# Kernel tuning notes

Hardware: AMD Instinct MI355X
Metric: run time of the kernel (lower is better)

Reference implementation:

```python
import jax, jax.numpy as jnp
import numpy as np

N, E = 50000, 800000
IN, C, H, EDIM = 128, 16, 8, 8  # in_channels, out_channels per head, heads, edge_dim
NEG_SLOPE = 0.2


def setup_inputs() -> dict:
    key = jax.random.key(0)
    ks = jax.random.split(key, 10)
    g = 1.0 / np.sqrt(IN)
    inp = {
        "x": jax.random.normal(ks[0], (N, IN), dtype=jnp.float32),
        "edge_index": jax.random.randint(ks[1], (2, E), 0, N, dtype=jnp.int64),
        "edge_attr": jax.random.normal(ks[2], (E, EDIM), dtype=jnp.float32),
        # GATv2Conv params (share_weights=False): lin_l, lin_r with bias, lin_edge no bias
        "W_l": jax.random.normal(ks[3], (IN, H * C), dtype=jnp.float32) * g,
        "b_l": jnp.zeros((H * C,), dtype=jnp.float32),
        "W_r": jax.random.normal(ks[4], (IN, H * C), dtype=jnp.float32) * g,
        "b_r": jnp.zeros((H * C,), dtype=jnp.float32),
        "W_e": jax.random.normal(ks[5], (EDIM, H * C), dtype=jnp.float32) * (1.0 / np.sqrt(EDIM)),
        "att": jax.random.normal(ks[6], (H, C), dtype=jnp.float32) * (1.0 / np.sqrt(C)),
        "bias": jnp.zeros((H * C,), dtype=jnp.float32),
    }
    return inp


def _gatv2_forward(x, edge_index, edge_attr, W_l, b_l, W_r, b_r, W_e, att, bias):
    n = x.shape[0]
    x_l = (x @ W_l + b_l).reshape(n, H, C)  # source transform
    x_r = (x @ W_r + b_r).reshape(n, H, C)  # target transform

    # add self-loops; edge_attr fill_value='mean' (PyG GATv2Conv default)
    loop = jnp.arange(n, dtype=edge_index.dtype)
    src = jnp.concatenate([edge_index[0], loop])
    dst = jnp.concatenate([edge_index[1], loop])
    loop_attr = jnp.broadcast_to(edge_attr.mean(axis=0, keepdims=True), (n, EDIM))
    e_attr = jnp.concatenate([edge_attr, loop_attr], axis=0)  # [E+N, EDIM]

    e_emb = (e_attr @ W_e).reshape(-1, H, C)  # [E+N, H, C]
    m = x_l[src] + x_r[dst] + e_emb          # gather per edge
    m = jax.nn.leaky_relu(m, NEG_SLOPE)
    logit = jnp.einsum("ehc,hc->eh", m, att)  # [E+N, H]

    # destination-grouped (scatter) softmax
    seg_max = jax.ops.segment_max(logit, dst, num_segments=n)
    expd = jnp.exp(logit - seg_max[dst])
    seg_sum = jax.ops.segment_sum(expd, dst, num_segments=n)
    alpha = expd / (seg_sum[dst] + 1e-16)     # [E+N, H]

    msg = alpha[:, :, None] * x_l[src]        # [E+N, H, C]
    out = jax.ops.segment_sum(msg, dst, num_segments=n)  # [N, H, C]
    return out.reshape(n, H * C) + bias       # concat heads + bias


def reference(x, edge_index, edge_attr, W_l, b_l, W_r, b_r, W_e, att, bias):
    return _gatv2_forward(x, edge_index, edge_attr, W_l, b_l, W_r, b_r, W_e, att, bias)
```

## Files before the change

kernel.cpp:

```cpp
#include <hip/hip_runtime.h>

#define NHEAD 8
#define CH    16
#define HC    128
#define INC   128
#define EDIM  8
#define NEG   0.2f

typedef _Float16 h8 __attribute__((ext_vector_type(8)));
typedef _Float16 h4 __attribute__((ext_vector_type(4)));
typedef _Float16 h2 __attribute__((ext_vector_type(2)));
typedef float    f4 __attribute__((ext_vector_type(4)));

__device__ __forceinline__ float lrelu(float v) { return v > 0.f ? v : NEG * v; }

__global__ void k_loop_emb(const float* __restrict__ attr_sum, const float* __restrict__ We,
                           const float* __restrict__ att, float* __restrict__ loop_emb,
                           _Float16* __restrict__ We16, _Float16* __restrict__ att16,
                           float invE) {
    int j = threadIdx.x;
    float acc = 0.f;
    #pragma unroll
    for (int d = 0; d < EDIM; ++d) {
        float w = We[d * HC + j];
        acc += attr_sum[d] * invE * w;
        We16[d * HC + j] = (_Float16)w;
    }
    loop_emb[j] = acc;
    att16[j] = (_Float16)att[j];
}

__global__ void k_packW(const float* __restrict__ Wl, const float* __restrict__ Wr,
                        _Float16* __restrict__ packed) {
    int id = blockIdx.x * blockDim.x + threadIdx.x;
    int l  = id & 63;
    int kb = (id >> 6) & 3;
    int t  = id >> 8;
    int col = t * 16 + (l & 15);
    const float* W = (col < HC) ? Wl : Wr;
    int c = col & 127;
    int kbase = kb * 32 + (l >> 4) * 8;
    _Float16* dst = packed + (size_t)id * 8;
    #pragma unroll
    for (int j = 0; j < 8; ++j) dst[j] = (_Float16)W[(size_t)(kbase + j) * HC + c];
}

__global__ __launch_bounds__(256) void k_gemm_mfma(
        const float* __restrict__ x, const _Float16* __restrict__ packed,
        const float* __restrict__ bl, const float* __restrict__ br,
        _Float16* __restrict__ xh, int N) {
    __shared__ _Float16 st[16][264];
    int nb0 = blockIdx.x * 128;
    int w  = threadIdx.x >> 6;
    int l  = threadIdx.x & 63;

    const h8* pk = (const h8*)packed;
    h8 bfrag[4][4];
    #pragma unroll
    for (int t4 = 0; t4 < 4; ++t4)
        #pragma unroll
        for (int kb = 0; kb < 4; ++kb)
            bfrag[t4][kb] = pk[(size_t)(((w * 4 + t4) * 4 + kb) * 64 + l)];

    float bv[4];
    int cl = l & 15;
    #pragma unroll
    for (int t4 = 0; t4 < 4; ++t4) {
        int col = w * 64 + t4 * 16 + cl;
        bv[t4] = (col < HC) ? bl[col] : br[col - HC];
    }

    int g = l >> 4;
    int r0 = g * 4;
    for (int mt = 0; mt < 8; ++mt) {
        int m0 = nb0 + mt * 16;
        if (m0 >= N) break;
        int row = m0 + cl; if (row >= N) row = N - 1;
        const float* xp = x + (size_t)row * INC + g * 8;
        h8 afrag[4];
        #pragma unroll
        for (int kb = 0; kb < 4; ++kb) {
            float4 u = *(const float4*)(xp + kb * 32);
            float4 v = *(const float4*)(xp + kb * 32 + 4);
            h8 a;
            a[0] = (_Float16)u.x; a[1] = (_Float16)u.y; a[2] = (_Float16)u.z; a[3] = (_Float16)u.w;
            a[4] = (_Float16)v.x; a[5] = (_Float16)v.y; a[6] = (_Float16)v.z; a[7] = (_Float16)v.w;
            afrag[kb] = a;
        }
        f4 acc[4];
        #pragma unroll
        for (int t4 = 0; t4 < 4; ++t4) { f4 z = {0.f, 0.f, 0.f, 0.f}; acc[t4] = z; }
        #pragma unroll
        for (int kb = 0; kb < 4; ++kb)
            #pragma unroll
            for (int t4 = 0; t4 < 4; ++t4)
                acc[t4] = __builtin_amdgcn_mfma_f32_16x16x32_f16(afrag[kb], bfrag[t4][kb], acc[t4], 0, 0, 0);
        #pragma unroll
        for (int t4 = 0; t4 < 4; ++t4) {
            int col = w * 64 + t4 * 16 + cl;
            #pragma unroll
            for (int j = 0; j < 4; ++j)
                st[r0 + j][col] = (_Float16)(acc[t4][j] + bv[t4]);
        }
        __syncthreads();
        #pragma unroll
        for (int q = 0; q < 2; ++q) {
            int cch = threadIdx.x + 256 * q;
            int r = cch >> 5, ch = (cch & 31) * 8;
            int node = m0 + r;
            if (node < N) *(h8*)(xh + (size_t)node * 256 + ch) = *(const h8*)&st[r][ch];
        }
        __syncthreads();
    }
}

__global__ void k_hist(const int* __restrict__ ei, int* __restrict__ cnt,
                       int* __restrict__ rank, int E) {
    int t = blockIdx.x * blockDim.x + threadIdx.x;
    if (t < E) rank[t] = atomicAdd(&cnt[ei[E + t]], 1);
}

__global__ void k_scan1(const int* __restrict__ cnt, int* __restrict__ off,
                        int* __restrict__ bsum, int N) {
    __shared__ int wpre[16];
    int i = blockIdx.x * 1024 + threadIdx.x;
    int lane = threadIdx.x & 63, wid = threadIdx.x >> 6;
    int v = (i < N) ? cnt[i] : 0;
    int s = v;
    #pragma unroll
    for (int d = 1; d < 64; d <<= 1) {
        int t = __shfl_up(s, d);
        if (lane >= d) s += t;
    }
    if (lane == 63) wpre[wid] = s;
    __syncthreads();
    if (threadIdx.x == 0) {
        int run = 0;
        #pragma unroll
        for (int q = 0; q < 16; ++q) { int t = wpre[q]; wpre[q] = run; run += t; }
        bsum[blockIdx.x] = run;
    }
    __syncthreads();
    if (i <= N) off[i] = wpre[wid] + s - v;
}

__global__ void k_scan2(const int* __restrict__ bsum, int* __restrict__ bsx, int nb) {
    int lane = threadIdx.x;
    int v = (lane < nb) ? bsum[lane] : 0;
    int s = v;
    #pragma unroll
    for (int d = 1; d < 64; d <<= 1) {
        int t = __shfl_up(s, d);
        if (lane >= d) s += t;
    }
    if (lane < nb) bsx[lane] = s - v;
}

__global__ void k_scatter(const int* __restrict__ ei, const float* __restrict__ ea,
                          const int* __restrict__ off, const int* __restrict__ bsx,
                          const int* __restrict__ rank,
                          int* __restrict__ esrc, h8* __restrict__ eac,
                          float* __restrict__ attr_sum, int E) {
    __shared__ float red[4][8];
    int t = blockIdx.x * blockDim.x + threadIdx.x;
    float av[8] = {0.f, 0.f, 0.f, 0.f, 0.f, 0.f, 0.f, 0.f};
    if (t < E) {
        int dst = ei[E + t];
        int pos = off[dst] + bsx[dst >> 10] + rank[t];
        esrc[pos] = ei[t];
        float4 a0 = *(const float4*)(ea + (size_t)t * EDIM);
        float4 a1 = *(const float4*)(ea + (size_t)t * EDIM + 4);
        av[0] = a0.x; av[1] = a0.y; av[2] = a0.z; av[3] = a0.w;
        av[4] = a1.x; av[5] = a1.y; av[6] = a1.z; av[7] = a1.w;
        h8 v;
        #pragma unroll
        for (int k = 0; k < 8; ++k) v[k] = (_Float16)av[k];
        eac[pos] = v;
    }
    #pragma unroll
    for (int m = 1; m < 64; m <<= 1) {
        #pragma unroll
        for (int k = 0; k < 8; ++k) av[k] += __shfl_xor(av[k], m);
    }
    int lane = threadIdx.x & 63, wid = threadIdx.x >> 6;
    if (lane == 0) {
        #pragma unroll
        for (int k = 0; k < 8; ++k) red[wid][k] = av[k];
    }
    __syncthreads();
    if (threadIdx.x < 8) {
        float s = red[0][threadIdx.x] + red[1][threadIdx.x] + red[2][threadIdx.x] + red[3][threadIdx.x];
        atomicAdd(&attr_sum[threadIdx.x], s);
    }
}

__global__ void k_gather(const int* __restrict__ esrc, const h8* __restrict__ eac,
                         const _Float16* __restrict__ We16, const _Float16* __restrict__ att16,
                         const float* __restrict__ att,
                         const _Float16* __restrict__ xh,
                         const float* __restrict__ loop_emb, const float* __restrict__ bias,
                         const int* __restrict__ off, const int* __restrict__ bsx,
                         float* __restrict__ out, int N) {
    int wave = (blockIdx.x * blockDim.x + threadIdx.x) >> 6;
    int lane = threadIdx.x & 63;
    if (wave >= N) return;
    int dst = __builtin_amdgcn_readfirstlane(wave);
    int half = lane >> 5;
    int l = lane & 31;
    int c0 = l * 4;

    h4 we4[EDIM];
    #pragma unroll
    for (int d = 0; d < EDIM; ++d) we4[d] = *(const h4*)(We16 + d * HC + c0);
    h2 attlo = *(const h2*)(att16 + c0);
    h2 atthi = *(const h2*)(att16 + c0 + 2);
    h4 xr4 = *(const h4*)(xh + (size_t)dst * 256 + HC + c0);
    float xr0 = (float)xr4[0], xr1 = (float)xr4[1], xr2f = (float)xr4[2], xr3 = (float)xr4[3];

    float acc0 = 0.f, acc1 = 0.f, acc2 = 0.f, acc3 = 0.f, segw = 0.f;

    {
        h4 xl4 = *(const h4*)(xh + (size_t)dst * 256 + c0);
        float x0 = (float)xl4[0], x1 = (float)xl4[1], x2 = (float)xl4[2], x3 = (float)xl4[3];
        float4 le = *(const float4*)(loop_emb + c0);
        float4 af = *(const float4*)(att + c0);
        float m0 = lrelu(x0 + xr0 + le.x);
        float m1 = lrelu(x1 + xr1 + le.y);
        float m2 = lrelu(x2 + xr2f + le.z);
        float m3 = lrelu(x3 + xr3 + le.w);
        float p = m0 * af.x + m1 * af.y + m2 * af.z + m3 * af.w;
        p += __shfl_xor(p, 1); p += __shfl_xor(p, 2);
        float w = half ? 0.f : __expf(p);
        segw += w; acc0 += w * x0; acc1 += w * x1; acc2 += w * x2; acc3 += w * x3;
    }

    int beg = off[dst] + bsx[dst >> 10];
    int end = off[dst + 1] + bsx[(dst + 1) >> 10];
    if (beg < end) {
        const h4 z4 = {};
        h4 ng4; ng4[0] = (_Float16)NEG; ng4[1] = (_Float16)NEG; ng4[2] = (_Float16)NEG; ng4[3] = (_Float16)NEG;
        int last = end - 1;
        int j0 = beg + half;     if (j0 > last) j0 = last;
        int j1 = beg + 2 + half; if (j1 > last) j1 = last;
        int j2 = beg + 4 + half; if (j2 > last) j2 = last;
        int sA = esrc[j0]; h8 aA = eac[j0];
        int sB = esrc[j1]; h8 aB = eac[j1];
        int sC = esrc[j2]; h8 aC = eac[j2];
        h4 xlA = *(const h4*)(xh + (size_t)sA * 256 + c0);
        h4 xlB = *(const h4*)(xh + (size_t)sB * 256 + c0);
        for (int i = beg; i < end; i += 2) {
            h4 xlC = *(const h4*)(xh + (size_t)sC * 256 + c0);
            int j3 = i + 6 + half; if (j3 > last) j3 = last;
            int sD = esrc[j3]; h8 aD = eac[j3];
            bool valid = (i + half) < end;
            h4 e4 = {};
            #pragma unroll
            for (int d = 0; d < EDIM; ++d) {
                h4 ad; ad[0] = aA[d]; ad[1] = aA[d]; ad[2] = aA[d]; ad[3] = aA[d];
                e4 += ad * we4[d];
            }
            h4 m4 = xlA + xr4 + e4;
            h4 mp = __builtin_elementwise_max(m4, z4);
            h4 mn = __builtin_elementwise_min(m4, z4);
            m4 = mp + mn * ng4;
            h2 mlo; mlo[0] = m4[0]; mlo[1] = m4[1];
            h2 mhi; mhi[0] = m4[2]; mhi[1] = m4[3];
#if __has_builtin(__builtin_amdgcn_fdot2)
            float p = __builtin_amdgcn_fdot2(mlo, attlo, 0.f, false);
            p = __builtin_amdgcn_fdot2(mhi, atthi, p, false);
#else
            float p = (float)m4[0] * (float)attlo[0] + (float)m4[1] * (float)attlo[1]
                    + (float)m4[2] * (float)atthi[0] + (float)m4[3] * (float)atthi[1];
#endif
            p += __shfl_xor(p, 1);
            p += __shfl_xor(p, 2);
            float w = valid ? __expf(p) : 0.f;
            segw += w;
            acc0 += w * (float)xlA[0];
            acc1 += w * (float)xlA[1];
            acc2 += w * (float)xlA[2];
            acc3 += w * (float)xlA[3];
            aA = aB; aB = aC; aC = aD;
            xlA = xlB; xlB = xlC;
            sC = sD;
        }
    }

    segw += __shfl_xor(segw, 32);
    acc0 += __shfl_xor(acc0, 32);
    acc1 += __shfl_xor(acc1, 32);
    acc2 += __shfl_xor(acc2, 32);
    acc3 += __shfl_xor(acc3, 32);

    if (half == 0) {
        float inv = 1.f / (segw + 1e-16f);
        float4 bv = *(const float4*)(bias + c0);
        float4 o;
        o.x = acc0 * inv + bv.x;
        o.y = acc1 * inv + bv.y;
        o.z = acc2 * inv + bv.z;
        o.w = acc3 * inv + bv.w;
        *(float4*)(out + (size_t)dst * HC + c0) = o;
    }
}

extern "C" void kernel_launch(void* const* d_in, const int* in_sizes, int n_in,
                              void* d_out, int out_size, void* d_ws, size_t ws_size,
                              hipStream_t stream) {
    int N = in_sizes[0] / INC;
    int E = in_sizes[1] / 2;
    const float* x    = (const float*)d_in[0];
    const int*   ei   = (const int*)d_in[1];
    const float* ea   = (const float*)d_in[2];
    const float* Wl   = (const float*)d_in[3];
    const float* bl   = (const float*)d_in[4];
    const float* Wr   = (const float*)d_in[5];
    const float* br   = (const float*)d_in[6];
    const float* We   = (const float*)d_in[7];
    const float* att  = (const float*)d_in[8];
    const float* bias = (const float*)d_in[9];
    float* out = (float*)d_out;

    _Float16* xh      = (_Float16*)d_ws;
    h8*       eac     = (h8*)(xh + (size_t)N * 256);
    float* attr_sum   = (float*)(eac + E);
    int*   cnt        = (int*)(attr_sum + 8);
    float* loop_emb   = (float*)(cnt + N);
    _Float16* packed  = (_Float16*)(loop_emb + HC);
    _Float16* We16    = packed + 32768;
    _Float16* att16   = We16 + 1024;
    int*   off        = (int*)(att16 + 128);
    int*   rank       = off + (N + 2);
    int*   esrc       = rank + E;
    int*   bsum       = esrc + E;
    int*   bsx        = bsum + 64;

    hipMemsetAsync(attr_sum, 0, (8 + (size_t)N) * sizeof(float), stream);

    k_packW<<<16, 256, 0, stream>>>(Wl, Wr, packed);
    k_gemm_mfma<<<(N + 127) / 128, 256, 0, stream>>>(x, packed, bl, br, xh, N);

    k_hist<<<(E + 255) / 256, 256, 0, stream>>>(ei, cnt, rank, E);
    int nb = (N + 1 + 1023) / 1024;
    k_scan1<<<nb, 1024, 0, stream>>>(cnt, off, bsum, N);
    k_scan2<<<1, 64, 0, stream>>>(bsum, bsx, nb);
    k_scatter<<<(E + 255) / 256, 256, 0, stream>>>(ei, ea, off, bsx, rank, esrc, eac, attr_sum, E);

    k_loop_emb<<<1, HC, 0, stream>>>(attr_sum, We, att, loop_emb, We16, att16, 1.0f / (float)E);

    k_gather<<<(N * 64 + 255) / 256, 256, 0, stream>>>(esrc, eac, We16, att16, att, xh,
                                                       loop_emb, bias, off, bsx, out, N);
}
```

Baseline: 187.9 us.

## Fuse GEMM with histogram, merge scan2 with loop-emb, widen gather to 4 edges per wave

```diff
diff --git a/kernel.cpp b/kernel.cpp
--- a/kernel.cpp
+++ b/kernel.cpp
@@ -14,20 +14,12 @@
 
 __device__ __forceinline__ float lrelu(float v) { return v > 0.f ? v : NEG * v; }
 
-__global__ void k_loop_emb(const float* __restrict__ attr_sum, const float* __restrict__ We,
-                           const float* __restrict__ att, float* __restrict__ loop_emb,
-                           _Float16* __restrict__ We16, _Float16* __restrict__ att16,
-                           float invE) {
-    int j = threadIdx.x;
-    float acc = 0.f;
-    #pragma unroll
-    for (int d = 0; d < EDIM; ++d) {
-        float w = We[d * HC + j];
-        acc += attr_sum[d] * invE * w;
-        We16[d * HC + j] = (_Float16)w;
-    }
-    loop_emb[j] = acc;
-    att16[j] = (_Float16)att[j];
+__device__ __forceinline__ float dot2(h2 a, h2 b, float c) {
+#if __has_builtin(__builtin_amdgcn_fdot2)
+    return __builtin_amdgcn_fdot2(a, b, c, false);
+#else
+    return c + (float)a[0] * (float)b[0] + (float)a[1] * (float)b[1];
+#endif
 }
 
 __global__ void k_packW(const float* __restrict__ Wl, const float* __restrict__ Wr,
@@ -45,79 +37,105 @@
     for (int j = 0; j < 8; ++j) dst[j] = (_Float16)W[(size_t)(kbase + j) * HC + c];
 }
 
-__global__ __launch_bounds__(256) void k_gemm_mfma(
+__global__ __launch_bounds__(256) void k_phase1(
         const float* __restrict__ x, const _Float16* __restrict__ packed,
         const float* __restrict__ bl, const float* __restrict__ br,
-        _Float16* __restrict__ xh, int N) {
+        _Float16* __restrict__ xh,
+        const int* __restrict__ ei, const float* __restrict__ ea,
+        int* __restrict__ cnt, int* __restrict__ rank, float* __restrict__ attr_sum,
+        int N, int E, int gemmBlocks) {
     __shared__ _Float16 st[16][264];
-    int nb0 = blockIdx.x * 128;
-    int w  = threadIdx.x >> 6;
-    int l  = threadIdx.x & 63;
-
-    const h8* pk = (const h8*)packed;
-    h8 bfrag[4][4];
-    #pragma unroll
-    for (int t4 = 0; t4 < 4; ++t4)
-        #pragma unroll
-        for (int kb = 0; kb < 4; ++kb)
-            bfrag[t4][kb] = pk[(size_t)(((w * 4 + t4) * 4 + kb) * 64 + l)];
-
-    float bv[4];
-    int cl = l & 15;
-    #pragma unroll
-    for (int t4 = 0; t4 < 4; ++t4) {
-        int col = w * 64 + t4 * 16 + cl;
-        bv[t4] = (col < HC) ? bl[col] : br[col - HC];
-    }
-
-    int g = l >> 4;
-    int r0 = g * 4;
-    for (int mt = 0; mt < 8; ++mt) {
-        int m0 = nb0 + mt * 16;
-        if (m0 >= N) break;
-        int row = m0 + cl; if (row >= N) row = N - 1;
-        const float* xp = x + (size_t)row * INC + g * 8;
-        h8 afrag[4];
-        #pragma unroll
-        for (int kb = 0; kb < 4; ++kb) {
-            float4 u = *(const float4*)(xp + kb * 32);
-            float4 v = *(const float4*)(xp + kb * 32 + 4);
-            h8 a;
-            a[0] = (_Float16)u.x; a[1] = (_Float16)u.y; a[2] = (_Float16)u.z; a[3] = (_Float16)u.w;
-            a[4] = (_Float16)v.x; a[5] = (_Float16)v.y; a[6] = (_Float16)v.z; a[7] = (_Float16)v.w;
-            afrag[kb] = a;
-        }
-        f4 acc[4];
-        #pragma unroll
-        for (int t4 = 0; t4 < 4; ++t4) { f4 z = {0.f, 0.f, 0.f, 0.f}; acc[t4] = z; }
-        #pragma unroll
-        for (int kb = 0; kb < 4; ++kb)
-            #pragma unroll
-            for (int t4 = 0; t4 < 4; ++t4)
-                acc[t4] = __builtin_amdgcn_mfma_f32_16x16x32_f16(afrag[kb], bfrag[t4][kb], acc[t4], 0, 0, 0);
+    __shared__ float red[4][8];
+
+    if ((int)blockIdx.x < gemmBlocks) {
+        int nb0 = blockIdx.x * 128;
+        int w  = threadIdx.x >> 6;
+        int l  = threadIdx.x & 63;
+
+        const h8* pk = (const h8*)packed;
+        h8 bfrag[4][4];
+        #pragma unroll
+        for (int t4 = 0; t4 < 4; ++t4)
+            #pragma unroll
+            for (int kb = 0; kb < 4; ++kb)
+                bfrag[t4][kb] = pk[(size_t)(((w * 4 + t4) * 4 + kb) * 64 + l)];
+
+        float bv[4];
+        int cl = l & 15;
         #pragma unroll
         for (int t4 = 0; t4 < 4; ++t4) {
             int col = w * 64 + t4 * 16 + cl;
-            #pragma unroll
-            for (int j = 0; j < 4; ++j)
-                st[r0 + j][col] = (_Float16)(acc[t4][j] + bv[t4]);
+            bv[t4] = (col < HC) ? bl[col] : br[col - HC];
+        }
+
+        int g = l >> 4;
+        int r0 = g * 4;
+        for (int mt = 0; mt < 8; ++mt) {
+            int m0 = nb0 + mt * 16;
+            if (m0 >= N) break;
+            int row = m0 + cl; if (row >= N) row = N - 1;
+            const float* xp = x + (size_t)row * INC + g * 8;
+            h8 afrag[4];
+            #pragma unroll
+            for (int kb = 0; kb < 4; ++kb) {
+                float4 u = *(const float4*)(xp + kb * 32);
+                float4 v = *(const float4*)(xp + kb * 32 + 4);
+                h8 a;
+                a[0] = (_Float16)u.x; a[1] = (_Float16)u.y; a[2] = (_Float16)u.z; a[3] = (_Float16)u.w;
+                a[4] = (_Float16)v.x; a[5] = (_Float16)v.y; a[6] = (_Float16)v.z; a[7] = (_Float16)v.w;
+                afrag[kb] = a;
+            }
+            f4 acc[4];
+            #pragma unroll
+            for (int t4 = 0; t4 < 4; ++t4) { f4 z = {0.f, 0.f, 0.f, 0.f}; acc[t4] = z; }
+            #pragma unroll
+            for (int kb = 0; kb < 4; ++kb)
+                #pragma unroll
+                for (int t4 = 0; t4 < 4; ++t4)
+                    acc[t4] = __builtin_amdgcn_mfma_f32_16x16x32_f16(afrag[kb], bfrag[t4][kb], acc[t4], 0, 0, 0);
+            #pragma unroll
+            for (int t4 = 0; t4 < 4; ++t4) {
+                int col = w * 64 + t4 * 16 + cl;
+                #pragma unroll
+                for (int j = 0; j < 4; ++j)
+                    st[r0 + j][col] = (_Float16)(acc[t4][j] + bv[t4]);
+            }
+            __syncthreads();
+            #pragma unroll
+            for (int q = 0; q < 2; ++q) {
+                int cch = threadIdx.x + 256 * q;
+                int r = cch >> 5, ch = (cch & 31) * 8;
+                int node = m0 + r;
+                if (node < N) *(h8*)(xh + (size_t)node * 256 + ch) = *(const h8*)&st[r][ch];
+            }
+            __syncthreads();
+        }
+    } else {
+        int t = (blockIdx.x - gemmBlocks) * 256 + threadIdx.x;
+        float av[8] = {0.f, 0.f, 0.f, 0.f, 0.f, 0.f, 0.f, 0.f};
+        if (t < E) {
+            rank[t] = atomicAdd(&cnt[ei[E + t]], 1);
+            float4 a0 = *(const float4*)(ea + (size_t)t * EDIM);
+            float4 a1 = *(const float4*)(ea + (size_t)t * EDIM + 4);
+            av[0] = a0.x; av[1] = a0.y; av[2] = a0.z; av[3] = a0.w;
+            av[4] = a1.x; av[5] = a1.y; av[6] = a1.z; av[7] = a1.w;
+        }
+        #pragma unroll
+        for (int m = 1; m < 64; m <<= 1) {
+            #pragma unroll
+            for (int k = 0; k < 8; ++k) av[k] += __shfl_xor(av[k], m);
+        }
+        int lane = threadIdx.x & 63, wid = threadIdx.x >> 6;
+        if (lane == 0) {
+            #pragma unroll
+            for (int k = 0; k < 8; ++k) red[wid][k] = av[k];
         }
         __syncthreads();
-        #pragma unroll
-        for (int q = 0; q < 2; ++q) {
-            int cch = threadIdx.x + 256 * q;
-            int r = cch >> 5, ch = (cch & 31) * 8;
-            int node = m0 + r;
-            if (node < N) *(h8*)(xh + (size_t)node * 256 + ch) = *(const h8*)&st[r][ch];
-        }
-        __syncthreads();
-    }
-}
-
-__global__ void k_hist(const int* __restrict__ ei, int* __restrict__ cnt,
-                       int* __restrict__ rank, int E) {
-    int t = blockIdx.x * blockDim.x + threadIdx.x;
-    if (t < E) rank[t] = atomicAdd(&cnt[ei[E + t]], 1);
+        if (threadIdx.x < 8) {
+            float s = red[0][threadIdx.x] + red[1][threadIdx.x] + red[2][threadIdx.x] + red[3][threadIdx.x];
+            atomicAdd(&attr_sum[threadIdx.x], s);
+        }
+    }
 }
 
 __global__ void k_scan1(const int* __restrict__ cnt, int* __restrict__ off,
@@ -144,163 +162,179 @@
     if (i <= N) off[i] = wpre[wid] + s - v;
 }
 
-__global__ void k_scan2(const int* __restrict__ bsum, int* __restrict__ bsx, int nb) {
-    int lane = threadIdx.x;
-    int v = (lane < nb) ? bsum[lane] : 0;
-    int s = v;
-    #pragma unroll
-    for (int d = 1; d < 64; d <<= 1) {
-        int t = __shfl_up(s, d);
-        if (lane >= d) s += t;
-    }
-    if (lane < nb) bsx[lane] = s - v;
+__global__ void k_scan2lo(const int* __restrict__ bsum, int* __restrict__ bsx, int nb,
+                          const float* __restrict__ attr_sum, const float* __restrict__ We,
+                          const float* __restrict__ att, float* __restrict__ loop_emb,
+                          _Float16* __restrict__ We16, _Float16* __restrict__ att16,
+                          float invE) {
+    int tid = threadIdx.x;
+    if (tid < 64) {
+        int v = (tid < nb) ? bsum[tid] : 0;
+        int s = v;
+        #pragma unroll
+        for (int d = 1; d < 64; d <<= 1) {
+            int t = __shfl_up(s, d);
+            if (tid >= d) s += t;
+        }
+        if (tid < nb) bsx[tid] = s - v;
+    } else if (tid < 192) {
+        int j = tid - 64;
+        float acc = 0.f;
+        #pragma unroll
+        for (int d = 0; d < EDIM; ++d) {
+            float w = We[d * HC + j];
+            acc += attr_sum[d] * invE * w;
+            We16[d * HC + j] = (_Float16)w;
+        }
+        loop_emb[j] = acc;
+        att16[j] = (_Float16)att[j];
+    }
 }
 
 __global__ void k_scatter(const int* __restrict__ ei, const float* __restrict__ ea,
                           const int* __restrict__ off, const int* __restrict__ bsx,
                           const int* __restrict__ rank,
-                          int* __restrict__ esrc, h8* __restrict__ eac,
-                          float* __restrict__ attr_sum, int E) {
-    __shared__ float red[4][8];
+                          int* __restrict__ esrc, h8* __restrict__ eac, int E) {
     int t = blockIdx.x * blockDim.x + threadIdx.x;
-    float av[8] = {0.f, 0.f, 0.f, 0.f, 0.f, 0.f, 0.f, 0.f};
-    if (t < E) {
-        int dst = ei[E + t];
-        int pos = off[dst] + bsx[dst >> 10] + rank[t];
-        esrc[pos] = ei[t];
-        float4 a0 = *(const float4*)(ea + (size_t)t * EDIM);
-        float4 a1 = *(const float4*)(ea + (size_t)t * EDIM + 4);
-        av[0] = a0.x; av[1] = a0.y; av[2] = a0.z; av[3] = a0.w;
-        av[4] = a1.x; av[5] = a1.y; av[6] = a1.z; av[7] = a1.w;
-        h8 v;
-        #pragma unroll
-        for (int k = 0; k < 8; ++k) v[k] = (_Float16)av[k];
-        eac[pos] = v;
-    }
-    #pragma unroll
-    for (int m = 1; m < 64; m <<= 1) {
-        #pragma unroll
-        for (int k = 0; k < 8; ++k) av[k] += __shfl_xor(av[k], m);
-    }
-    int lane = threadIdx.x & 63, wid = threadIdx.x >> 6;
-    if (lane == 0) {
-        #pragma unroll
-        for (int k = 0; k < 8; ++k) red[wid][k] = av[k];
-    }
-    __syncthreads();
-    if (threadIdx.x < 8) {
-        float s = red[0][threadIdx.x] + red[1][threadIdx.x] + red[2][threadIdx.x] + red[3][threadIdx.x];
-        atomicAdd(&attr_sum[threadIdx.x], s);
-    }
-}
-
-__global__ void k_gather(const int* __restrict__ esrc, const h8* __restrict__ eac,
-                         const _Float16* __restrict__ We16, const _Float16* __restrict__ att16,
-                         const float* __restrict__ att,
-                         const _Float16* __restrict__ xh,
-                         const float* __restrict__ loop_emb, const float* __restrict__ bias,
-                         const int* __restrict__ off, const int* __restrict__ bsx,
-                         float* __restrict__ out, int N) {
+    if (t >= E) return;
+    int dst = ei[E + t];
+    int pos = off[dst] + bsx[dst >> 10] + rank[t];
+    esrc[pos] = ei[t];
+    float4 a0 = *(const float4*)(ea + (size_t)t * EDIM);
+    float4 a1 = *(const float4*)(ea + (size_t)t * EDIM + 4);
+    h8 v;
+    v[0] = (_Float16)a0.x; v[1] = (_Float16)a0.y; v[2] = (_Float16)a0.z; v[3] = (_Float16)a0.w;
+    v[4] = (_Float16)a1.x; v[5] = (_Float16)a1.y; v[6] = (_Float16)a1.z; v[7] = (_Float16)a1.w;
+    eac[pos] = v;
+}
+
+__global__ __launch_bounds__(256) void k_gather(
+        const int* __restrict__ esrc, const h8* __restrict__ eac,
+        const _Float16* __restrict__ We16, const _Float16* __restrict__ att16,
+        const float* __restrict__ attf, const _Float16* __restrict__ xh,
+        const float* __restrict__ loop_emb, const float* __restrict__ bias,
+        const int* __restrict__ off, const int* __restrict__ bsx,
+        float* __restrict__ out, int N) {
     int wave = (blockIdx.x * blockDim.x + threadIdx.x) >> 6;
     int lane = threadIdx.x & 63;
     if (wave >= N) return;
     int dst = __builtin_amdgcn_readfirstlane(wave);
-    int half = lane >> 5;
-    int l = lane & 31;
-    int c0 = l * 4;
-
-    h4 we4[EDIM];
-    #pragma unroll
-    for (int d = 0; d < EDIM; ++d) we4[d] = *(const h4*)(We16 + d * HC + c0);
-    h2 attlo = *(const h2*)(att16 + c0);
-    h2 atthi = *(const h2*)(att16 + c0 + 2);
-    h4 xr4 = *(const h4*)(xh + (size_t)dst * 256 + HC + c0);
-    float xr0 = (float)xr4[0], xr1 = (float)xr4[1], xr2f = (float)xr4[2], xr3 = (float)xr4[3];
-
-    float acc0 = 0.f, acc1 = 0.f, acc2 = 0.f, acc3 = 0.f, segw = 0.f;
+    int qid = lane >> 4;
+    int l   = lane & 15;
+    int c0  = l * 8;
+
+    h8 we8[EDIM];
+    #pragma unroll
+    for (int d = 0; d < EDIM; ++d) we8[d] = *(const h8*)(We16 + d * HC + c0);
+    h2 att2[4];
+    #pragma unroll
+    for (int k = 0; k < 4; ++k) att2[k] = *(const h2*)(att16 + c0 + 2 * k);
+    h8 xr8 = *(const h8*)(xh + (size_t)dst * 256 + HC + c0);
+
+    const h8 z8 = {};
+    h8 ng8;
+    #pragma unroll
+    for (int k = 0; k < 8; ++k) ng8[k] = (_Float16)NEG;
+
+    float accv[8] = {0.f, 0.f, 0.f, 0.f, 0.f, 0.f, 0.f, 0.f};
+    float segw = 0.f;
+
+    auto PROC = [&](h8 a8, h8 x8, bool cond) {
+        h8 e8 = {};
+        #pragma unroll
+        for (int d = 0; d < EDIM; ++d) {
+            h8 ad = {a8[d], a8[d], a8[d], a8[d], a8[d], a8[d], a8[d], a8[d]};
+            e8 += ad * we8[d];
+        }
+        h8 m8 = x8 + xr8 + e8;
+        h8 mp = __builtin_elementwise_max(m8, z8);
+        h8 mn = __builtin_elementwise_min(m8, z8);
+        m8 = mp + mn * ng8;
+        float p = 0.f;
+        #pragma unroll
+        for (int k = 0; k < 4; ++k) {
+            h2 mm; mm[0] = m8[2 * k]; mm[1] = m8[2 * k + 1];
+            p = dot2(mm, att2[k], p);
+        }
+        p += __shfl_xor(p, 1);
+        float w = cond ? __expf(p) : 0.f;
+        segw += w;
+        #pragma unroll
+        for (int k = 0; k < 8; ++k) accv[k] += w * (float)x8[k];
+    };
 
     {
-        h4 xl4 = *(const h4*)(xh + (size_t)dst * 256 + c0);
-        float x0 = (float)xl4[0], x1 = (float)xl4[1], x2 = (float)xl4[2], x3 = (float)xl4[3];
-        float4 le = *(const float4*)(loop_emb + c0);
-        float4 af = *(const float4*)(att + c0);
-        float m0 = lrelu(x0 + xr0 + le.x);
-        float m1 = lrelu(x1 + xr1 + le.y);
-        float m2 = lrelu(x2 + xr2f + le.z);
-        float m3 = lrelu(x3 + xr3 + le.w);
-        float p = m0 * af.x + m1 * af.y + m2 * af.z + m3 * af.w;
-        p += __shfl_xor(p, 1); p += __shfl_xor(p, 2);
-        float w = half ? 0.f : __expf(p);
-        segw += w; acc0 += w * x0; acc1 += w * x1; acc2 += w * x2; acc3 += w * x3;
+        h8 xl8 = *(const h8*)(xh + (size_t)dst * 256 + c0);
+        f4 le0 = *(const f4*)(loop_emb + c0), le1 = *(const f4*)(loop_emb + c0 + 4);
+        f4 af0 = *(const f4*)(attf + c0),     af1 = *(const f4*)(attf + c0 + 4);
+        float le[8] = {le0[0], le0[1], le0[2], le0[3], le1[0], le1[1], le1[2], le1[3]};
+        float af[8] = {af0[0], af0[1], af0[2], af0[3], af1[0], af1[1], af1[2], af1[3]};
+        float xf[8];
+        float p = 0.f;
+        #pragma unroll
+        for (int k = 0; k < 8; ++k) {
+            xf[k] = (float)xl8[k];
+            p += lrelu(xf[k] + (float)xr8[k] + le[k]) * af[k];
+        }
+        p += __shfl_xor(p, 1);
+        float w = (qid == 0) ? __expf(p) : 0.f;
+        segw += w;
+        #pragma unroll
+        for (int k = 0; k < 8; ++k) accv[k] += w * xf[k];
     }
 
     int beg = off[dst] + bsx[dst >> 10];
     int end = off[dst + 1] + bsx[(dst + 1) >> 10];
     if (beg < end) {
-        const h4 z4 = {};
-        h4 ng4; ng4[0] = (_Float16)NEG; ng4[1] = (_Float16)NEG; ng4[2] = (_Float16)NEG; ng4[3] = (_Float16)NEG;
         int last = end - 1;
-        int j0 = beg + half;     if (j0 > last) j0 = last;
-        int j1 = beg + 2 + half; if (j1 > last) j1 = last;
-        int j2 = beg + 4 + half; if (j2 > last) j2 = last;
-        int sA = esrc[j0]; h8 aA = eac[j0];
-        int sB = esrc[j1]; h8 aB = eac[j1];
-        int sC = esrc[j2]; h8 aC = eac[j2];
-        h4 xlA = *(const h4*)(xh + (size_t)sA * 256 + c0);
-        h4 xlB = *(const h4*)(xh + (size_t)sB * 256 + c0);
-        for (int i = beg; i < end; i += 2) {
-            h4 xlC = *(const h4*)(xh + (size_t)sC * 256 + c0);
-            int j3 = i + 6 + half; if (j3 > last) j3 = last;
-            int sD = esrc[j3]; h8 aD = eac[j3];
-            bool valid = (i + half) < end;
-            h4 e4 = {};
-            #pragma unroll
-            for (int d = 0; d < EDIM; ++d) {
-                h4 ad; ad[0] = aA[d]; ad[1] = aA[d]; ad[2] = aA[d]; ad[3] = aA[d];
-                e4 += ad * we4[d];
-            }
-            h4 m4 = xlA + xr4 + e4;
-            h4 mp = __builtin_elementwise_max(m4, z4);
-            h4 mn = __builtin_elementwise_min(m4, z4);
-            m4 = mp + mn * ng4;
-            h2 mlo; mlo[0] = m4[0]; mlo[1] = m4[1];
-            h2 mhi; mhi[0] = m4[2]; mhi[1] = m4[3];
-#if __has_builtin(__builtin_amdgcn_fdot2)
-            float p = __builtin_amdgcn_fdot2(mlo, attlo, 0.f, false);
-            p = __builtin_amdgcn_fdot2(mhi, atthi, p, false);
-#else
-            float p = (float)m4[0] * (float)attlo[0] + (float)m4[1] * (float)attlo[1]
-                    + (float)m4[2] * (float)atthi[0] + (float)m4[3] * (float)atthi[1];
-#endif
-            p += __shfl_xor(p, 1);
-            p += __shfl_xor(p, 2);
-            float w = valid ? __expf(p) : 0.f;
-            segw += w;
-            acc0 += w * (float)xlA[0];
-            acc1 += w * (float)xlA[1];
-            acc2 += w * (float)xlA[2];
-            acc3 += w * (float)xlA[3];
-            aA = aB; aB = aC; aC = aD;
-            xlA = xlB; xlB = xlC;
-            sC = sD;
-        }
-    }
-
-    segw += __shfl_xor(segw, 32);
-    acc0 += __shfl_xor(acc0, 32);
-    acc1 += __shfl_xor(acc1, 32);
-    acc2 += __shfl_xor(acc2, 32);
-    acc3 += __shfl_xor(acc3, 32);
-
-    if (half == 0) {
+        int j;
+        j = beg + qid;          if (j > last) j = last;
+        int sU = esrc[j]; h8 aU = eac[j];
+        j = beg + 4 + qid;      if (j > last) j = last;
+        int sV = esrc[j]; h8 aV = eac[j];
+        h8 xU = *(const h8*)(xh + (size_t)sU * 256 + c0);
+        h8 xV = *(const h8*)(xh + (size_t)sV * 256 + c0);
+        j = beg + 8 + qid;      if (j > last) j = last;
+        int sP = esrc[j];
+        j = beg + 12 + qid;     if (j > last) j = last;
+        int sQ = esrc[j];
+        for (int i = beg; i < end; i += 8) {
+            PROC(aU, xU, (i + qid) < end);
+            {
+                int jx = i + 8 + qid;  if (jx > last) jx = last;
+                xU = *(const h8*)(xh + (size_t)sP * 256 + c0);
+                aU = eac[jx];
+                int jf = i + 16 + qid; if (jf > last) jf = last;
+                sP = esrc[jf];
+            }
+            PROC(aV, xV, (i + 4 + qid) < end);
+            {
+                int jx = i + 12 + qid; if (jx > last) jx = last;
+                xV = *(const h8*)(xh + (size_t)sQ * 256 + c0);
+                aV = eac[jx];
+                int jf = i + 20 + qid; if (jf > last) jf = last;
+                sQ = esrc[jf];
+            }
+        }
+    }
+
+    segw += __shfl_xor(segw, 16); segw += __shfl_xor(segw, 32);
+    #pragma unroll
+    for (int k = 0; k < 8; ++k) {
+        accv[k] += __shfl_xor(accv[k], 16);
+        accv[k] += __shfl_xor(accv[k], 32);
+    }
+
+    if (qid == 0) {
         float inv = 1.f / (segw + 1e-16f);
-        float4 bv = *(const float4*)(bias + c0);
-        float4 o;
-        o.x = acc0 * inv + bv.x;
-        o.y = acc1 * inv + bv.y;
-        o.z = acc2 * inv + bv.z;
-        o.w = acc3 * inv + bv.w;
-        *(float4*)(out + (size_t)dst * HC + c0) = o;
+        f4 b0 = *(const f4*)(bias + c0), b1 = *(const f4*)(bias + c0 + 4);
+        f4 o0, o1;
+        o0[0] = accv[0] * inv + b0[0]; o0[1] = accv[1] * inv + b0[1];
+        o0[2] = accv[2] * inv + b0[2]; o0[3] = accv[3] * inv + b0[3];
+        o1[0] = accv[4] * inv + b1[0]; o1[1] = accv[5] * inv + b1[1];
+        o1[2] = accv[6] * inv + b1[2]; o1[3] = accv[7] * inv + b1[3];
+        *(f4*)(out + (size_t)dst * HC + c0)     = o0;
+        *(f4*)(out + (size_t)dst * HC + c0 + 4) = o1;
     }
 }
 
@@ -338,15 +372,18 @@
     hipMemsetAsync(attr_sum, 0, (8 + (size_t)N) * sizeof(float), stream);
 
     k_packW<<<16, 256, 0, stream>>>(Wl, Wr, packed);
-    k_gemm_mfma<<<(N + 127) / 128, 256, 0, stream>>>(x, packed, bl, br, xh, N);
-
-    k_hist<<<(E + 255) / 256, 256, 0, stream>>>(ei, cnt, rank, E);
+
+    int gemmBlocks = (N + 127) / 128;
+    int histBlocks = (E + 255) / 256;
+    k_phase1<<<gemmBlocks + histBlocks, 256, 0, stream>>>(x, packed, bl, br, xh,
+                                                          ei, ea, cnt, rank, attr_sum,
+                                                          N, E, gemmBlocks);
+
     int nb = (N + 1 + 1023) / 1024;
     k_scan1<<<nb, 1024, 0, stream>>>(cnt, off, bsum, N);
-    k_scan2<<<1, 64, 0, stream>>>(bsum, bsx, nb);
-    k_scatter<<<(E + 255) / 256, 256, 0, stream>>>(ei, ea, off, bsx, rank, esrc, eac, attr_sum, E);
-
-    k_loop_emb<<<1, HC, 0, stream>>>(attr_sum, We, att, loop_emb, We16, att16, 1.0f / (float)E);
+    k_scan2lo<<<1, 256, 0, stream>>>(bsum, bsx, nb, attr_sum, We, att,
+                                     loop_emb, We16, att16, 1.0f / (float)E);
+    k_scatter<<<histBlocks, 256, 0, stream>>>(ei, ea, off, bsx, rank, esrc, eac, E);
 
     k_gather<<<(N * 64 + 255) / 256, 256, 0, stream>>>(esrc, eac, We16, att16, att, xh,
                                                        loop_emb, bias, off, bsx, out, N);
```

After: 167.4 us. 10.9% less time.
